# Optimization experiments

Hardware: AMD Instinct MI355X
Metric: run time of the kernel (lower is better)

Reference implementation:

```python
import jax, jax.numpy as jnp
import numpy as np
from jax import lax

N = 200; E = 3200; HID = 64; NH = 16; OUT = 2 * HID; CAT = NH * OUT  # CAT = 2048
ALPHA = 0.2


def _gat(h, e_attr, adj, n2n, W, a_s, a_d, a_e, We, concat):
    # edge-feature-aware GAT head: logits from Wh_i, Wh_j and projected node2node feats
    Nn = h.shape[0]
    Wh = h @ W                                       # [N, out]
    ee = ((n2n @ We) @ a_e).reshape(Nn, Nn)          # [N, N] edge-feature term
    logits = jax.nn.leaky_relu((Wh @ a_s)[:, None] + (Wh @ a_d)[None, :] + ee,
                               negative_slope=ALPHA)
    logits = jnp.where(adj > 0, logits, -1e9)        # mask to graph structure
    att = jax.nn.softmax(logits, axis=1)
    h2 = att @ Wh
    if concat:
        h2 = jax.nn.elu(h2)
    return h2, jax.nn.elu(e_attr @ We)               # updated node + edge features


def _edge_pool(x, eidx, e, w, b):
    # static-shape edge pooling: score edges, gate nodes by mean incident score
    src, dst = eidx[0], eidx[1]
    s = jax.nn.sigmoid(jnp.concatenate([x[src], x[dst], e], axis=1) @ w + b)  # [E]
    deg = jax.ops.segment_sum(jnp.ones_like(s), src, num_segments=x.shape[0])
    ns = jax.ops.segment_sum(s, src, num_segments=x.shape[0]) / (deg + 1e-6)
    return x * ns[:, None], e * s[:, None]


def _gpool(x, w, b):
    # GlobalAttention: gate_nn = Linear+Sigmoid, softmax over nodes, weighted sum
    gate = jax.nn.softmax(jax.nn.sigmoid(x @ w + b), axis=0)  # [N, 1]
    return jnp.sum(gate * x, axis=0, keepdims=True)           # [1, D]


def _adj_n2n(Nn, eidx, eattr):
    # vectorized version of the per-edge Python loop in _get_adj_node2node
    src, dst = eidx[0], eidx[1]
    adj = jnp.zeros((Nn, Nn), eattr.dtype).at[src, dst].set(1.0)
    n2n = jnp.zeros((Nn * Nn, eattr.shape[1]), eattr.dtype).at[src * Nn + dst].set(eattr)
    return adj, n2n


def _lstm_dir(x, Wih, Whh, b):
    # one LSTM direction over seq x [T, Din] (PyTorch i,f,g,o gate order)
    Hh = Whh.shape[1]
    def step(carry, xt):
        h, c = carry
        g = xt @ Wih.T + h @ Whh.T + b
        i, f, gg, o = jnp.split(g, 4)
        c = jax.nn.sigmoid(f) * c + jax.nn.sigmoid(i) * jnp.tanh(gg)
        h = jax.nn.sigmoid(o) * jnp.tanh(c)
        return (h, c), h
    (_, _), ys = lax.scan(step, (jnp.zeros(Hh, x.dtype), jnp.zeros(Hh, x.dtype)), x)
    return ys


def setup_inputs():
    key = jax.random.key(0)
    ks = iter(jax.random.split(key, 64))
    def rn(shape, scale=0.05):
        return jax.random.normal(next(ks), shape, jnp.float32) * scale
    inp = {}
    for g in (1, 2):
        eidx = jax.random.randint(next(ks), (2, E), 0, N)
        eattr = rn((E, HID), 1.0)
        adj, n2n = _adj_n2n(N, eidx, eattr)
        inp['features%d' % g] = rn((N, HID), 1.0)
        inp['edge_index%d' % g] = eidx
        inp['edgesAttr%d' % g] = eattr
        inp['adjacency%d' % g] = adj
        inp['node2node%d' % g] = n2n
    inp.update(dict(
        W_h=rn((HID, HID)),
        W_gat=rn((NH, HID, OUT)), a_src=rn((NH, OUT)), a_dst=rn((NH, OUT)),
        a_e=rn((NH, OUT)), We_gat=rn((NH, HID, OUT)),
        W_out=rn((CAT, OUT)), ao_src=rn((OUT,)), ao_dst=rn((OUT,)), ao_e=rn((OUT,)),
        We_out=rn((CAT, OUT)),
        ep1_w=rn((3 * CAT,)), ep1_b=rn(()),
        ep2_w=rn((3 * OUT,)), ep2_b=rn(()),
        g1_w=rn((HID, 1)), g1_b=rn((1,)),
        g2_w=rn((CAT, 1)), g2_b=rn((1,)),
        g3_w=rn((OUT, 1)), g3_b=rn((1,)),
        Wih0=rn((2, 512, 35 * HID)), Whh0=rn((2, 512, 128)), b0=rn((2, 512)),
        Wih1=rn((2, 512, 256)), Whh1=rn((2, 512, 128)), b1=rn((2, 512)),
        fc_w=rn((256, 2)), fc_b=rn((2,)),
    ))
    return inp


def reference(features1, features2, edge_index1, edge_index2, edgesAttr1, edgesAttr2,
              adjacency1, adjacency2, node2node1, node2node2,
              W_h, W_gat, a_src, a_dst, a_e, We_gat,
              W_out, ao_src, ao_dst, ao_e, We_out,
              ep1_w, ep1_b, ep2_w, ep2_b,
              g1_w, g1_b, g2_w, g2_b, g3_w, g3_b,
              Wih0, Whh0, b0, Wih1, Whh1, b1, fc_w, fc_b):
    def graph(feat, eidx, eattr, adj, n2n):
        h = jax.nn.elu(feat @ W_h)                              # SingleNodeAttentionLayer
        hs = [_gpool(h, g1_w, g1_b)]
        outs = [_gat(h, eattr, adj, n2n, W_gat[i], a_src[i], a_dst[i], a_e[i],
                     We_gat[i], True) for i in range(NH)]
        h = jnp.concatenate([o[0] for o in outs], axis=1)       # [N, 2048]
        eattr = jnp.concatenate([o[1] for o in outs], axis=1)   # [E, 2048]
        h, eattr = _edge_pool(h, eidx, eattr, ep1_w, ep1_b)
        hs.append(_gpool(h, g2_w, g2_b))
        adj2, n2n2 = _adj_n2n(h.shape[0], eidx, eattr)          # dense [N*N, 2048]
        h, eattr = _gat(h, eattr, adj2, n2n2, W_out, ao_src, ao_dst, ao_e, We_out, False)
        h, eattr = _edge_pool(h, eidx, eattr, ep2_w, ep2_b)
        hs.append(_gpool(h, g3_w, g3_b))
        return jnp.concatenate(hs, axis=1)                      # [1, 35*HID]

    h1 = graph(features1, edge_index1, edgesAttr1, adjacency1, node2node1)
    h2 = graph(features2, edge_index2, edgesAttr2, adjacency2, node2node2)
    x = jnp.concatenate([h1, h2], axis=0)                       # seq [2, 2240]
    for Wih, Whh, b in ((Wih0, Whh0, b0), (Wih1, Whh1, b1)):
        f = _lstm_dir(x, Wih[0], Whh[0], b[0])
        r = _lstm_dir(x[::-1], Wih[1], Whh[1], b[1])[::-1]
        x = jnp.concatenate([f, r], axis=1)                     # [2, 256]
    logits = x[-1] @ fc_w + fc_b
    return jax.nn.softmax(logits)[None, :]                      # [1, nclass]
```

## Files before the change

kernel.cpp:

```cpp
#include <hip/hip_runtime.h>
#include <math.h>

#define DI static __device__ __forceinline__

DI float eluf(float x){ return x > 0.f ? x : expm1f(x); }
DI float lreluf(float x){ return x > 0.f ? x : 0.2f*x; }
DI float sigmf(float x){ return 1.f/(1.f+expf(-x)); }

typedef unsigned short u16;
typedef unsigned int   u32;
typedef __attribute__((ext_vector_type(8))) short short8_t;
typedef __attribute__((ext_vector_type(4))) float f32x4;

DI u16 bf16rne(float f){
  u32 u = __float_as_uint(f);
  u += 0x7fffu + ((u>>16)&1u);
  return (u16)(u>>16);
}

DI f32x4 bmfma(short8_t a, short8_t b, f32x4 c){
  return __builtin_amdgcn_mfma_f32_16x16x32_bf16(a, b, c, 0, 0, 0);
}

constexpr int N=200, E=3200, HID=64, NH=16, OUTD=128, CAT=2048, SEQD=2240;

constexpr int OH0   = 0;
constexpr int OWH   = OH0 + N*HID;
constexpr int OASN  = OWH + NH*N*OUTD;
constexpr int OADN  = OASN + NH*N;
constexpr int OH1   = OADN + NH*N;
constexpr int OXW1  = OH1 + N*CAT;
constexpr int OXW2  = OXW1 + 256;
constexpr int OEW1  = OXW2 + 256;
constexpr int OS1   = OEW1 + E;
constexpr int ODEG1 = OS1 + E;
constexpr int OSS1  = ODEG1 + 256;
constexpr int ORAW1 = OSS1 + 256;
constexpr int OWH2  = ORAW1 + 256;
constexpr int OAS2  = OWH2 + N*OUTD;
constexpr int OAD2  = OAS2 + 256;
constexpr int OEWV  = OAD2 + 256;
constexpr int OH2B  = OEWV + E;
constexpr int OXS2  = OH2B + N*OUTD;
constexpr int OXD2  = OXS2 + 256;
constexpr int ODEG2 = OXD2 + 256;
constexpr int OSS2  = ODEG2 + 256;
constexpr int ORAW2 = OSS2 + 256;
constexpr int ORAW3 = ORAW2 + 256;
constexpr int PGF   = ORAW3 + 256;
constexpr int GLOBF = 10624;
constexpr int TOTF  = GLOBF + 2*PGF;

__device__ float G_F[TOTF];
__device__ float G_E2PART[(size_t)2*2*E*OUTD];
__device__ float G_EDOTH[2*NH*E];
__device__ float G_WHHT[2*2*128*512];
__device__ int   G_PIDX[2*N*N];
__device__ __attribute__((aligned(16))) u16 G_WGAT_T[NH*OUTD*HID];
__device__ __attribute__((aligned(16))) u16 G_WOUT_T[OUTD*CAT];
__device__ __attribute__((aligned(16))) u16 G_EATTR_BF[2*E*HID];

DI float* gf(int g){ return G_F + GLOBF + (size_t)g*PGF; }
DI float* gwe_ae(){ return G_F; }
DI float* gv_e(){ return G_F + 1024; }
DI float* gy0(){ return G_F + 3072; }
DI float* gy1(){ return G_F + 3584; }
DI float* gxseq(){ return G_F + 4096; }
DI float* gxg(){ return G_F + 8576; }
DI int*   gpidx(int g){ return G_PIDX + g*N*N; }

struct GraphIn {
  const float *feat, *eattr, *adj, *n2n;
  const int   *eidx;
};

struct Params {
  GraphIn g[2];
  const float *W_h, *W_gat, *a_src, *a_dst, *a_e, *We_gat;
  const float *W_out, *ao_src, *ao_dst, *ao_e, *We_out;
  const float *ep1_w, *ep1_b, *ep2_w, *ep2_b;
  const float *g1_w, *g1_b, *g2_w, *g2_b, *g3_w, *g3_b;
  const float *Wih0, *Whh0, *b0, *Wih1, *Whh1, *b1, *fc_w, *fc_b;
  float *out;
};

constexpr int ZPG  = 2*E + 1024;
constexpr int IB_Z = (2*ZPG+255)/256;
constexpr int IB_C = (2*N*N+255)/256;
constexpr int IB_D = (2*2*512*128)/256;
constexpr int IB_E = (NH*HID+CAT+3)/4;
constexpr int IB_H = (2*N+3)/4;
constexpr int IB_W1 = (NH*OUTD*HID)/256;
constexpr int IB_W2 = (OUTD*CAT)/256;
constexpr int IB_EA = (2*E*HID)/256;
__global__ void k_init(Params P){
  int b = blockIdx.x, tid = threadIdx.x;
  if (b < IB_Z){
    int i = b*256 + tid;
    if (i < 2*ZPG){
      int g = i/ZPG, r = i%ZPG;
      int addr = r<E ? OEW1+r : (r<2*E ? OEWV+(r-E) :
                 (r<2*E+512 ? ODEG1+(r-2*E) : ODEG2+(r-2*E-512)));
      gf(g)[addr] = 0.f;
    }
  } else if (b < IB_Z+IB_C){
    int i = (b-IB_Z)*256 + tid; if (i < 2*N*N) G_PIDX[i] = -1;
  } else if (b < IB_Z+IB_C+IB_D){
    int idx = (b-IB_Z-IB_C)*256 + tid;
    int l = idx >> 17;
    int r = idx & 131071;
    int d = r >> 16;
    int r2 = r & 65535;
    int gate = r2 & 511;
    int k = r2 >> 9;
    const float* Whh = l ? P.Whh1 : P.Whh0;
    G_WHHT[idx] = Whh[((size_t)d*512+gate)*128 + k];
  } else if (b < IB_Z+IB_C+IB_D+IB_E){
    int gid = (b-IB_Z-IB_C-IB_D)*4 + (tid>>6);
    int lane = tid & 63;
    if (gid < NH*HID){
      int h = gid/HID, c = gid%HID;
      const float* W = P.We_gat + (size_t)(h*HID+c)*OUTD;
      const float* a = P.a_e + h*OUTD;
      float acc = 0.f;
      for (int o=lane;o<OUTD;o+=64) acc += W[o]*a[o];
      for (int off=32;off>0;off>>=1) acc += __shfl_down(acc,off);
      if (lane==0) gwe_ae()[gid] = acc;
    } else if (gid < NH*HID+CAT){
      int c = gid - NH*HID;
      const float* W = P.We_out + (size_t)c*OUTD;
      float acc = 0.f;
      for (int o=lane;o<OUTD;o+=64) acc += W[o]*P.ao_e[o];
      for (int off=32;off>0;off>>=1) acc += __shfl_down(acc,off);
      if (lane==0) gv_e()[c] = acc;
    }
  } else if (b < IB_Z+IB_C+IB_D+IB_E+IB_H){
    int unit = (b-IB_Z-IB_C-IB_D-IB_E)*4 + (tid>>6);
    if (unit >= 2*N) return;
    int g = unit / N, n = unit % N, c = tid & 63;
    const float* feat = P.g[g].feat;
    float acc = 0.f;
    for (int k=0;k<HID;k++) acc += feat[n*HID+k]*P.W_h[k*HID+c];
    float v = eluf(acc);
    float* f = gf(g);
    f[OH0 + n*HID + c] = v;
    float r = v*P.g1_w[c];
    for (int off=32;off>0;off>>=1) r += __shfl_down(r,off);
    if (c==0) f[ORAW1+n] = r;
  } else if (b < IB_Z+IB_C+IB_D+IB_E+IB_H+IB_W1){
    int i = (b-(IB_Z+IB_C+IB_D+IB_E+IB_H))*256 + tid;
    int h = i>>13, o = (i>>6)&127, c = i&63;
    G_WGAT_T[i] = bf16rne(P.We_gat[(size_t)(h*HID+c)*OUTD + o]);
  } else if (b < IB_Z+IB_C+IB_D+IB_E+IB_H+IB_W1+IB_W2){
    int i = (b-(IB_Z+IB_C+IB_D+IB_E+IB_H+IB_W1))*256 + tid;
    int n = i>>11, q = i&2047;
    G_WOUT_T[i] = bf16rne(P.We_out[(size_t)q*OUTD + n]);
  } else {
    int i = (b-(IB_Z+IB_C+IB_D+IB_E+IB_H+IB_W1+IB_W2))*256 + tid;
    int g = i >= E*HID ? 1 : 0;
    G_EATTR_BF[i] = bf16rne(P.g[g].eattr[i - g*E*HID]);
  }
}

__global__ void k_edoth(Params P){
  int unit = blockIdx.x*4 + (threadIdx.x>>6);
  int lane = threadIdx.x & 63;
  int g = unit >= E ? 1 : 0;
  int e = unit - g*E;
  float val = P.g[g].eattr[(size_t)e*HID + lane];
  const float* wa = gwe_ae();
  float* eo = G_EDOTH + (size_t)g*NH*E + e;
  for (int h=0; h<NH; h++){
    float p = val * wa[h*HID + lane];
    for (int off=32; off>0; off>>=1) p += __shfl_down(p, off);
    if (lane==0) eo[(size_t)h*E] = p;
  }
}

__global__ void k_Wh(Params P){
  int n = blockIdx.x, h = blockIdx.y, g = blockIdx.z, o = threadIdx.x;
  float* f = gf(g);
  if (h == NH){
    if (n != 0) return;
    __shared__ float att[N];
    __shared__ float sb[128];
    for (int j = o; j < N; j += 128) att[j] = sigmf(f[ORAW1+j] + P.g1_b[0]);
    __syncthreads();
    float m = -3e38f;
    for (int j = o; j < N; j += 128) m = fmaxf(m, att[j]);
    sb[o] = m; __syncthreads();
    for (int s=64;s>0;s>>=1){ if (o<s) sb[o]=fmaxf(sb[o],sb[o+s]); __syncthreads(); }
    m = sb[0]; __syncthreads();
    float ss = 0.f;
    for (int j = o; j < N; j += 128){ float e = expf(att[j]-m); ss += e; }
    sb[o] = ss; __syncthreads();
    for (int s=64;s>0;s>>=1){ if (o<s) sb[o]+=sb[o+s]; __syncthreads(); }
    float inv = 1.f/sb[0]; __syncthreads();
    for (int j = o; j < N; j += 128) att[j] = expf(att[j]-m)*inv;
    __syncthreads();
    if (o < HID){
      float acc = 0.f;
      for (int j=0;j<N;j++) acc += att[j]*f[OH0 + j*HID + o];
      gxseq()[g*SEQD + o] = acc;
    }
    return;
  }
  __shared__ float hs[HID];
  __shared__ float sred[128], dred[128];
  if (o < HID) hs[o] = f[OH0 + n*HID + o];
  __syncthreads();
  const float* W = P.W_gat + (size_t)h*HID*OUTD + o;
  float acc = 0.f;
  for (int c=0;c<HID;c++) acc += hs[c]*W[(size_t)c*OUTD];
  f[OWH + ((size_t)h*N + n)*OUTD + o] = acc;
  sred[o] = acc*P.a_src[h*OUTD+o];
  dred[o] = acc*P.a_dst[h*OUTD+o];
  __syncthreads();
  for (int s=64;s>0;s>>=1){ if (o<s){ sred[o]+=sred[o+s]; dred[o]+=dred[o+s]; } __syncthreads(); }
  if (o==0){ f[OASN+h*N+n]=sred[0]; f[OADN+h*N+n]=dred[0]; }
}

__global__ void k_att1(Params P){
  int nb = blockIdx.x, h = blockIdx.y, g = blockIdx.z, tid = threadIdx.x;
  int n0 = nb*4;
  __shared__ float z[4][N];
  __shared__ float red[128];
  __shared__ float sinv[4];
  float* f = gf(g);
  const float* adj = P.g[g].adj;
  const int* pidx = gpidx(g);
  const float* edoth = G_EDOTH + ((size_t)g*NH + h)*E;
  const float* adn = f + OADN + h*N;
  for (int i=0;i<4;i++){
    float asn = f[OASN + h*N + n0+i];
    for (int j = tid; j < N; j += 128){
      float a = adj[(n0+i)*N + j];
      float zz;
      if (a > 0.f){
        int p = pidx[(n0+i)*N + j];
        float ee = (p >= 0) ? edoth[p] : 0.f;
        zz = lreluf(asn + adn[j] + ee);
      } else zz = -1e9f;
      z[i][j] = zz;
    }
  }
  __syncthreads();
  for (int i=0;i<4;i++){
    float m = -3e38f;
    for (int j = tid; j < N; j += 128) m = fmaxf(m, z[i][j]);
    red[tid] = m; __syncthreads();
    for (int s=64;s>0;s>>=1){ if (tid<s) red[tid]=fmaxf(red[tid],red[tid+s]); __syncthreads(); }
    m = red[0]; __syncthreads();
    float ssum = 0.f;
    for (int j = tid; j < N; j += 128){ float e = expf(z[i][j]-m); z[i][j]=e; ssum += e; }
    red[tid] = ssum; __syncthreads();
    for (int s=64;s>0;s>>=1){ if (tid<s) red[tid]+=red[tid+s]; __syncthreads(); }
    if (tid==0) sinv[i] = 1.f/red[0];
    __syncthreads();
  }
  const float* wh = f + OWH + (size_t)h*N*OUTD;
  float a0=0.f,a1=0.f,a2=0.f,a3=0.f;
  for (int j=0;j<N;j++){
    float w = wh[(size_t)j*OUTD + tid];
    a0 += z[0][j]*w; a1 += z[1][j]*w; a2 += z[2][j]*w; a3 += z[3][j]*w;
  }
  f[OH1 + (size_t)(n0+0)*CAT + h*OUTD + tid] = eluf(a0*sinv[0]);
  f[OH1 + (size_t)(n0+1)*CAT + h*OUTD + tid] = eluf(a1*sinv[1]);
  f[OH1 + (size_t)(n0+2)*CAT + h*OUTD + tid] = eluf(a2*sinv[2]);
  f[OH1 + (size_t)(n0+3)*CAT + h*OUTD + tid] = eluf(a3*sinv[3]);
}

__global__ void k_xw1(Params P){
  int n = blockIdx.x, g = blockIdx.y, tid = threadIdx.x;
  __shared__ float s1b[256], s2b[256], s3b[256];
  float* f = gf(g);
  const float* x = f + OH1 + (size_t)n*CAT;
  float a1 = 0.f, a2 = 0.f, a3 = 0.f;
  for (int c = tid; c < CAT; c += 256){
    float xv = x[c];
    a1 += xv*P.ep1_w[c];
    a2 += xv*P.ep1_w[CAT+c];
    a3 += xv*P.g2_w[c];
  }
  s1b[tid]=a1; s2b[tid]=a2; s3b[tid]=a3; __syncthreads();
  for (int s=128;s>0;s>>=1){
    if (tid<s){ s1b[tid]+=s1b[tid+s]; s2b[tid]+=s2b[tid+s]; s3b[tid]+=s3b[tid+s]; }
    __syncthreads();
  }
  if (tid==0){ f[OXW1+n]=s1b[0]; f[OXW2+n]=s2b[0]; f[ORAW2+n]=s3b[0]; }
}

__global__ void k_s1(Params P){
  int e = blockIdx.x*256 + threadIdx.x, g = blockIdx.y;
  if (e >= E) return;
  float* f = gf(g);
  const int* ei = P.g[g].eidx;
  int s = ei[e], d = ei[E+e];
  float v = sigmf(f[OXW1+s] + f[OXW2+d] + f[OEW1+e] + P.ep1_b[0]);
  f[OS1+e] = v;
  atomicAdd(&f[OSS1+s], v);
  atomicAdd(&f[ODEG1+s], 1.f);
}

__global__ void k_pairs(Params P){
  int e = blockIdx.x*256 + threadIdx.x, g = blockIdx.y;
  if (e >= E) return;
  const int* ei = P.g[g].eidx;
  atomicMax(&gpidx(g)[ei[e]*N + ei[E+e]], e);
}

__global__ void k_gpool_out(Params P, int xoff, int D, int odeg, int rawoff,
                            const float* b, int outoff){
  int cb = blockIdx.x, g = blockIdx.y, tid = threadIdx.x;
  __shared__ float att[N];
  __shared__ float sb[256];
  float* f = gf(g);
  for (int n = tid; n < N; n += 256){
    float sc = f[odeg+256+n]/(f[odeg+n]+1e-6f);
    att[n] = sigmf(f[rawoff+n]*sc + b[0]);
  }
  __syncthreads();
  float m = -3e38f;
  for (int n = tid; n < N; n += 256) m = fmaxf(m, att[n]);
  sb[tid] = m; __syncthreads();
  for (int s=128;s>0;s>>=1){ if (tid<s) sb[tid]=fmaxf(sb[tid],sb[tid+s]); __syncthreads(); }
  m = sb[0]; __syncthreads();
  float ss = 0.f;
  for (int n = tid; n < N; n += 256){ float e = expf(att[n]-m); ss += e; }
  sb[tid] = ss; __syncthreads();
  for (int s=128;s>0;s>>=1){ if (tid<s) sb[tid]+=sb[tid+s]; __syncthreads(); }
  float inv = 1.f/sb[0]; __syncthreads();
  for (int n = tid; n < N; n += 256){
    float sc = f[odeg+256+n]/(f[odeg+n]+1e-6f);
    att[n] = expf(att[n]-m)*inv*sc;
  }
  __syncthreads();
  int c = cb*256 + tid;
  if (c < D){
    const float* x = f + xoff;
    float acc = 0.f;
    for (int n=0;n<N;n++) acc += att[n]*x[(size_t)n*D + c];
    gxseq()[g*SEQD + outoff + c] = acc;
  }
}

__global__ void k_Wh2(Params P){
  int n = blockIdx.x, g = blockIdx.y, tid = threadIdx.x;
  int kq = tid >> 7, o = tid & 127;
  __shared__ float hrow[4][128];
  __shared__ float part[4][128];
  __shared__ float sr[128], dr[128];
  float* f = gf(g);
  const float* x = f + OH1 + (size_t)n*CAT;
  float acc = 0.f;
  for (int cc=0; cc<4; cc++){
    int c0 = kq*512 + cc*128;
    __syncthreads();
    hrow[kq][o] = x[c0 + o];
    __syncthreads();
    const float* W = P.W_out + (size_t)c0*OUTD + o;
    for (int j=0;j<128;j++) acc += hrow[kq][j]*W[(size_t)j*OUTD];
  }
  part[kq][o] = acc;
  __syncthreads();
  if (kq==0){
    float ns = f[OSS1+n]/(f[ODEG1+n]+1e-6f);
    float a = part[0][o]+part[1][o]+part[2][o]+part[3][o];
    float v = a*ns;
    f[OWH2 + (size_t)n*OUTD + o] = v;
    sr[o] = v*P.ao_src[o];
    dr[o] = v*P.ao_dst[o];
  }
  __syncthreads();
  for (int s=64;s>0;s>>=1){
    if (tid<s){ sr[tid]+=sr[tid+s]; dr[tid]+=dr[tid+s]; }
    __syncthreads();
  }
  if (tid==0){ f[OAS2+n]=sr[0]; f[OAD2+n]=dr[0]; }
}

__global__ void k_att2(Params P){
  int n = blockIdx.x, g = blockIdx.y, tid = threadIdx.x;
  __shared__ float z[N];
  __shared__ float red[128];
  __shared__ float dred[128];
  __shared__ float gred[128];
  float* f = gf(g);
  const float* adj = P.g[g].adj;
  const int* pidx = gpidx(g);
  float asn = f[OAS2+n];
  const float* adn = f + OAD2;
  for (int j = tid; j < N; j += 128){
    float a = adj[n*N + j];
    float zz;
    if (a > 0.f){
      int p = pidx[n*N + j];
      float ee = (p >= 0) ? f[OEWV+p]*f[OS1+p] : 0.f;
      zz = lreluf(asn + adn[j] + ee);
    } else zz = -1e9f;
    z[j] = zz;
  }
  __syncthreads();
  float m = -3e38f;
  for (int j = tid; j < N; j += 128) m = fmaxf(m, z[j]);
  red[tid] = m; __syncthreads();
  for (int s=64;s>0;s>>=1){ if (tid<s) red[tid]=fmaxf(red[tid],red[tid+s]); __syncthreads(); }
  m = red[0]; __syncthreads();
  float ssum = 0.f;
  for (int j = tid; j < N; j += 128){ float e = expf(z[j]-m); z[j]=e; ssum += e; }
  red[tid] = ssum; __syncthreads();
  for (int s=64;s>0;s>>=1){ if (tid<s) red[tid]+=red[tid+s]; __syncthreads(); }
  float inv = 1.f/red[0]; __syncthreads();
  const float* wh = f + OWH2;
  float acc = 0.f;
  for (int j=0;j<N;j++){
    float w = z[j];
    if (w != 0.f) acc += w * wh[(size_t)j*OUTD + tid];
  }
  float v = acc*inv;
  f[OH2B + (size_t)n*OUTD + tid] = v;
  red[tid]  = v*P.ep2_w[tid];
  dred[tid] = v*P.ep2_w[OUTD+tid];
  gred[tid] = v*P.g3_w[tid];
  __syncthreads();
  for (int s=64;s>0;s>>=1){
    if (tid<s){ red[tid]+=red[tid+s]; dred[tid]+=dred[tid+s]; gred[tid]+=gred[tid+s]; }
    __syncthreads();
  }
  if (tid==0){ f[OXS2+n]=red[0]; f[OXD2+n]=dred[0]; f[ORAW3+n]=gred[0]; }
}

__global__ __launch_bounds__(256) void k_e2p_mfma(Params P){
  int eb = blockIdx.x, hg = blockIdx.y, g = blockIdx.z;
  int tid = threadIdx.x;
  int wave = tid>>6, lane = tid&63, l16 = lane&15, l4 = lane>>4;
  __shared__ __attribute__((aligned(16))) u16 Tlds[16*512];
  int e0 = eb*16;
  int nt0 = wave*2;
  const u16* ea = G_EATTR_BF + ((size_t)g*E + e0)*HID;
  short8_t afrag0 = *(const short8_t*)(ea + l16*HID + l4*8);
  short8_t afrag1 = *(const short8_t*)(ea + l16*HID + 32 + l4*8);
  f32x4 acc0 = {0.f,0.f,0.f,0.f}, acc1 = {0.f,0.f,0.f,0.f};
  float ew1p[4] = {0.f,0.f,0.f,0.f};
  float ewvp[4] = {0.f,0.f,0.f,0.f};
  for (int pass=0; pass<2; pass++){
    if (pass) __syncthreads();
    for (int hh=0; hh<4; hh++){
      int h = hg*8 + pass*4 + hh;
      const u16* Wg = G_WGAT_T + (size_t)h*OUTD*HID;
      #pragma unroll
      for (int nn=0; nn<2; nn++){
        int nt = nt0 + nn;
        const u16* Wgn = Wg + (size_t)(nt*16 + l16)*HID + l4*8;
        f32x4 d = {0.f,0.f,0.f,0.f};
        d = bmfma(afrag0, *(const short8_t*)Wgn, d);
        d = bmfma(afrag1, *(const short8_t*)(Wgn+32), d);
        int qg = h*OUTD + nt*16 + l16;
        float w1 = P.ep1_w[2*CAT + qg];
        float wv = gv_e()[qg];
        int qloc = hh*128 + nt*16 + l16;
        #pragma unroll
        for (int r=0;r<4;r++){
          float v = d[r] > 0.f ? d[r] : expm1f(d[r]);
          ew1p[r] += v*w1;
          ewvp[r] += v*wv;
          float o = __shfl_xor(v, 1);
          if (!(lane&1)){
            u32 pk = (u32)bf16rne(v) | ((u32)bf16rne(o)<<16);
            int row = l4*4 + r;
            int byte = (row*1024 + qloc*2) ^ ((row&7)<<4);
            *(u32*)((char*)Tlds + byte) = pk;
          }
        }
      }
    }
    __syncthreads();
    const u16* Wo0 = G_WOUT_T + (size_t)(nt0*16 + l16)*CAT      + hg*1024 + pass*512 + l4*8;
    const u16* Wo1 = G_WOUT_T + (size_t)(nt0*16 + 16 + l16)*CAT + hg*1024 + pass*512 + l4*8;
    #pragma unroll 4
    for (int ks=0; ks<16; ks++){
      int byte = (l16*1024 + ks*64 + l4*16) ^ ((l16&7)<<4);
      short8_t af = *(const short8_t*)((const char*)Tlds + byte);
      acc0 = bmfma(af, *(const short8_t*)(Wo0 + ks*32), acc0);
      acc1 = bmfma(af, *(const short8_t*)(Wo1 + ks*32), acc1);
    }
  }
  float* f = gf(g);
  #pragma unroll
  for (int r=0;r<4;r++){
    float a = ew1p[r], b2 = ewvp[r];
    a += __shfl_xor(a, 1); b2 += __shfl_xor(b2, 1);
    a += __shfl_xor(a, 2); b2 += __shfl_xor(b2, 2);
    a += __shfl_xor(a, 4); b2 += __shfl_xor(b2, 4);
    a += __shfl_xor(a, 8); b2 += __shfl_xor(b2, 8);
    if (l16==0){
      int e = e0 + l4*4 + r;
      atomicAdd(&f[OEW1+e], a);
      atomicAdd(&f[OEWV+e], b2);
    }
  }
  float* dst = G_E2PART + (((size_t)hg*2 + g)*E + e0)*OUTD;
  #pragma unroll
  for (int r=0;r<4;r++){
    int e = l4*4 + r;
    dst[(size_t)e*OUTD + nt0*16 + l16]      = acc0[r];
    dst[(size_t)e*OUTD + nt0*16 + 16 + l16] = acc1[r];
  }
}

constexpr int TE2 = 16;
__global__ void k_ew2fin(Params P){
  int e0 = blockIdx.x*TE2, g = blockIdx.y, tid = threadIdx.x;
  __shared__ float lred[2][TE2];
  float* f = gf(g);
  float w2 = P.ep2_w[2*OUTD + tid];
  int lane = tid & 63, wvi = tid >> 6;
  for (int e=0;e<TE2;e++){
    const float* src = G_E2PART + ((size_t)g*E + e0 + e)*OUTD + tid;
    float a = 0.f;
    for (int h=0;h<2;h++) a += src[(size_t)h*2*E*OUTD];
    float v = eluf(f[OS1+e0+e]*a) * w2;
    for (int off=32;off>0;off>>=1) v += __shfl_down(v,off);
    if (lane==0) lred[wvi][e]=v;
  }
  __syncthreads();
  if (tid < TE2){
    int e = e0 + tid;
    float ew2 = lred[0][tid]+lred[1][tid];
    const int* ei = P.g[g].eidx;
    int s = ei[e], d = ei[E+e];
    float v = sigmf(f[OXS2+s] + f[OXD2+d] + ew2 + P.ep2_b[0]);
    atomicAdd(&f[OSS2+s], v);
    atomicAdd(&f[ODEG2+s], 1.f);
  }
}

__global__ void k_lstm_xg(Params P, int layer){
  int gid = blockIdx.x*4 + (threadIdx.x>>6);
  int lane = threadIdx.x & 63;
  int t = gid >> 10;
  int rem = gid & 1023;
  int d = rem >> 9;
  int gate = rem & 511;
  const float* Wih = layer ? P.Wih1 : P.Wih0;
  const float* bb  = layer ? P.b1   : P.b0;
  const float* xin = layer ? gy0()  : gxseq();
  int Din = layer ? 256 : SEQD;
  const float* x = xin + t*Din;
  const float* Wr = Wih + ((size_t)d*512 + gate)*Din;
  float acc = 0.f;
  for (int k=lane; k<Din; k+=64) acc += x[k]*Wr[k];
  for (int off=32; off>0; off>>=1) acc += __shfl_down(acc, off);
  if (lane==0) gxg()[(t*2 + d)*512 + gate] = acc + bb[d*512 + gate];
}

__global__ void k_lstm_rec(Params P, int layer){
  int d = blockIdx.x, tid = threadIdx.x;
  float* yout = layer ? gy1() : gy0();
  const float* T = G_WHHT + (size_t)(layer*2 + d)*128*512;
  __shared__ float h[128], c[128], gbuf[512];
  if (tid < 128){ h[tid]=0.f; c[tid]=0.f; }
  __syncthreads();
  for (int s=0;s<2;s++){
    int t = (d==0) ? s : 1-s;
    float acc = gxg()[(t*2 + d)*512 + tid];
    for (int k=0;k<128;k++) acc += h[k]*T[(size_t)k*512 + tid];
    gbuf[tid] = acc;
    __syncthreads();
    if (tid < 128){
      float ii = sigmf(gbuf[tid]);
      float ff = sigmf(gbuf[128+tid]);
      float gg = tanhf(gbuf[256+tid]);
      float oo = sigmf(gbuf[384+tid]);
      float cn = ff*c[tid] + ii*gg;
      c[tid] = cn;
      float hn = oo*tanhf(cn);
      h[tid] = hn;
      yout[t*256 + d*128 + tid] = hn;
    }
    __syncthreads();
  }
}

__global__ void k_final(Params P){
  int tid = threadIdx.x;
  __shared__ float sb[256], sb2[256];
  const float* x = gy1() + 256;
  sb[tid]  = x[tid]*P.fc_w[tid*2+0];
  sb2[tid] = x[tid]*P.fc_w[tid*2+1];
  __syncthreads();
  for (int s=128;s>0;s>>=1){ if (tid<s){ sb[tid]+=sb[tid+s]; sb2[tid]+=sb2[tid+s]; } __syncthreads(); }
  if (tid==0){
    float l0 = sb[0] + P.fc_b[0];
    float l1 = sb2[0] + P.fc_b[1];
    float m = fmaxf(l0,l1);
    float e0 = expf(l0-m), e1 = expf(l1-m), inv = 1.f/(e0+e1);
    P.out[0] = e0*inv;
    P.out[1] = e1*inv;
  }
}

extern "C" void kernel_launch(void* const* d_in, const int* in_sizes, int n_in,
                              void* d_out, int out_size, void* d_ws, size_t ws_size,
                              hipStream_t stream){
  Params P;
  for (int g=0; g<2; ++g){
    int b = g*5;
    P.g[g].feat  = (const float*)d_in[b+0];
    P.g[g].eidx  = (const int*)d_in[b+1];
    P.g[g].eattr = (const float*)d_in[b+2];
    P.g[g].adj   = (const float*)d_in[b+3];
    P.g[g].n2n   = (const float*)d_in[b+4];
  }
  P.W_h   = (const float*)d_in[10];
  P.W_gat = (const float*)d_in[11];
  P.a_src = (const float*)d_in[12];
  P.a_dst = (const float*)d_in[13];
  P.a_e   = (const float*)d_in[14];
  P.We_gat= (const float*)d_in[15];
  P.W_out = (const float*)d_in[16];
  P.ao_src= (const float*)d_in[17];
  P.ao_dst= (const float*)d_in[18];
  P.ao_e  = (const float*)d_in[19];
  P.We_out= (const float*)d_in[20];
  P.ep1_w = (const float*)d_in[21];
  P.ep1_b = (const float*)d_in[22];
  P.ep2_w = (const float*)d_in[23];
  P.ep2_b = (const float*)d_in[24];
  P.g1_w  = (const float*)d_in[25];
  P.g1_b  = (const float*)d_in[26];
  P.g2_w  = (const float*)d_in[27];
  P.g2_b  = (const float*)d_in[28];
  P.g3_w  = (const float*)d_in[29];
  P.g3_b  = (const float*)d_in[30];
  P.Wih0  = (const float*)d_in[31];
  P.Whh0  = (const float*)d_in[32];
  P.b0    = (const float*)d_in[33];
  P.Wih1  = (const float*)d_in[34];
  P.Whh1  = (const float*)d_in[35];
  P.b1    = (const float*)d_in[36];
  P.fc_w  = (const float*)d_in[37];
  P.fc_b  = (const float*)d_in[38];
  P.out   = (float*)d_out;

  k_init <<<dim3(IB_Z+IB_C+IB_D+IB_E+IB_H+IB_W1+IB_W2+IB_EA), 256, 0, stream>>>(P);
  k_pairs<<<dim3((E+255)/256,2), 256, 0, stream>>>(P);
  k_edoth<<<dim3(2*E/4), 256, 0, stream>>>(P);
  k_e2p_mfma<<<dim3(E/16, 2, 2), 256, 0, stream>>>(P);
  k_Wh   <<<dim3(N,NH+1,2), 128, 0, stream>>>(P);
  k_att1 <<<dim3(N/4,NH,2),128, 0, stream>>>(P);
  k_xw1  <<<dim3(N,2),    256, 0, stream>>>(P);
  k_s1   <<<dim3((E+255)/256,2), 256, 0, stream>>>(P);
  k_gpool_out<<<dim3(8,2), 256, 0, stream>>>(P, OH1, CAT, ODEG1, ORAW2, P.g2_b, HID);
  k_Wh2  <<<dim3(N,2),    512, 0, stream>>>(P);
  k_att2 <<<dim3(N,2),    128, 0, stream>>>(P);
  k_ew2fin<<<dim3(E/TE2,2),128, 0, stream>>>(P);
  k_gpool_out<<<dim3(1,2), 256, 0, stream>>>(P, OH2B, OUTD, ODEG2, ORAW3, P.g3_b, HID+CAT);

  k_lstm_xg <<<dim3(512), 256, 0, stream>>>(P, 0);
  k_lstm_rec<<<dim3(2),   512, 0, stream>>>(P, 0);
  k_lstm_xg <<<dim3(512), 256, 0, stream>>>(P, 1);
  k_lstm_rec<<<dim3(2),   512, 0, stream>>>(P, 1);
  k_final<<<dim3(1), 256, 0, stream>>>(P);
}
```

Measured before the change: 387.5 us.

## Retile edge projection MFMA kernel to 32 edges and 4 head groups

The edge-projection MFMA kernel now processes 32 edges per block over 4 head groups of 4 heads each, replacing 16 edges over 2 groups of 8. Each weight fragment is reused across two edge tiles, and the output-weight loads are register double-buffered ahead of the MFMAs. The partial-sum buffer grows to 4 slices, which the finalize kernel now sums. Separately, k_edoth is rewritten as a small LDS-tiled dot-product kernel in place of per-head wave shuffle reductions. The cost is a larger LDS footprint and more partial sums to write and reduce.

```diff
diff --git a/kernel.cpp b/kernel.cpp
--- a/kernel.cpp
+++ b/kernel.cpp
@@ -51,8 +51,8 @@
 constexpr int GLOBF = 10624;
 constexpr int TOTF  = GLOBF + 2*PGF;
 
-__device__ float G_F[TOTF];
-__device__ float G_E2PART[(size_t)2*2*E*OUTD];
+__device__ __attribute__((aligned(16))) float G_F[TOTF];
+__device__ float G_E2PART[(size_t)4*2*E*OUTD];
 __device__ float G_EDOTH[2*NH*E];
 __device__ float G_WHHT[2*2*128*512];
 __device__ int   G_PIDX[2*N*N];
@@ -163,18 +163,24 @@
 }
 
 __global__ void k_edoth(Params P){
-  int unit = blockIdx.x*4 + (threadIdx.x>>6);
-  int lane = threadIdx.x & 63;
-  int g = unit >= E ? 1 : 0;
-  int e = unit - g*E;
-  float val = P.g[g].eattr[(size_t)e*HID + lane];
-  const float* wa = gwe_ae();
-  float* eo = G_EDOTH + (size_t)g*NH*E + e;
-  for (int h=0; h<NH; h++){
-    float p = val * wa[h*HID + lane];
-    for (int off=32; off>0; off>>=1) p += __shfl_down(p, off);
-    if (lane==0) eo[(size_t)h*E] = p;
-  }
+  int b = blockIdx.x, tid = threadIdx.x;
+  int g = b / (E/16);
+  int e0 = (b % (E/16)) * 16;
+  __shared__ float ea[16][HID+1];
+  __shared__ float wa[16][HID+1];
+  {
+    int row = tid >> 4, c0 = (tid & 15)*4;
+    float4 v = *(const float4*)&P.g[g].eattr[(size_t)(e0+row)*HID + c0];
+    ea[row][c0]=v.x; ea[row][c0+1]=v.y; ea[row][c0+2]=v.z; ea[row][c0+3]=v.w;
+    float4 w = *(const float4*)&gwe_ae()[row*HID + c0];
+    wa[row][c0]=w.x; wa[row][c0+1]=w.y; wa[row][c0+2]=w.z; wa[row][c0+3]=w.w;
+  }
+  __syncthreads();
+  int h = tid >> 4, el = tid & 15;
+  float acc = 0.f;
+  #pragma unroll
+  for (int c=0;c<HID;c++) acc += ea[el][c]*wa[h][c];
+  G_EDOTH[((size_t)g*NH + h)*E + e0 + el] = acc;
 }
 
 __global__ void k_Wh(Params P){
@@ -434,77 +440,96 @@
   int eb = blockIdx.x, hg = blockIdx.y, g = blockIdx.z;
   int tid = threadIdx.x;
   int wave = tid>>6, lane = tid&63, l16 = lane&15, l4 = lane>>4;
-  __shared__ __attribute__((aligned(16))) u16 Tlds[16*512];
-  int e0 = eb*16;
+  __shared__ __attribute__((aligned(16))) u16 Tlds[32*512];
+  int e0 = eb*32;
   int nt0 = wave*2;
   const u16* ea = G_EATTR_BF + ((size_t)g*E + e0)*HID;
-  short8_t afrag0 = *(const short8_t*)(ea + l16*HID + l4*8);
-  short8_t afrag1 = *(const short8_t*)(ea + l16*HID + 32 + l4*8);
-  f32x4 acc0 = {0.f,0.f,0.f,0.f}, acc1 = {0.f,0.f,0.f,0.f};
-  float ew1p[4] = {0.f,0.f,0.f,0.f};
-  float ewvp[4] = {0.f,0.f,0.f,0.f};
-  for (int pass=0; pass<2; pass++){
-    if (pass) __syncthreads();
-    for (int hh=0; hh<4; hh++){
-      int h = hg*8 + pass*4 + hh;
-      const u16* Wg = G_WGAT_T + (size_t)h*OUTD*HID;
+  short8_t af00 = *(const short8_t*)(ea + l16*HID + l4*8);
+  short8_t af01 = *(const short8_t*)(ea + l16*HID + 32 + l4*8);
+  short8_t af10 = *(const short8_t*)(ea + (16+l16)*HID + l4*8);
+  short8_t af11 = *(const short8_t*)(ea + (16+l16)*HID + 32 + l4*8);
+  float ew1p0[4] = {0.f,0.f,0.f,0.f}, ewvp0[4] = {0.f,0.f,0.f,0.f};
+  float ew1p1[4] = {0.f,0.f,0.f,0.f}, ewvp1[4] = {0.f,0.f,0.f,0.f};
+  for (int hh=0; hh<4; hh++){
+    int h = hg*4 + hh;
+    const u16* Wg = G_WGAT_T + (size_t)h*OUTD*HID;
+    #pragma unroll
+    for (int nn=0; nn<2; nn++){
+      int nt = nt0 + nn;
+      const u16* Wgn = Wg + (size_t)(nt*16 + l16)*HID + l4*8;
+      short8_t wg0 = *(const short8_t*)Wgn;
+      short8_t wg1 = *(const short8_t*)(Wgn + 32);
+      f32x4 d0 = {0.f,0.f,0.f,0.f}, d1 = {0.f,0.f,0.f,0.f};
+      d0 = bmfma(af00, wg0, d0);
+      d1 = bmfma(af10, wg0, d1);
+      d0 = bmfma(af01, wg1, d0);
+      d1 = bmfma(af11, wg1, d1);
+      int qg = h*OUTD + nt*16 + l16;
+      float w1 = P.ep1_w[2*CAT + qg];
+      float wv = gv_e()[qg];
+      int qloc = hh*128 + nt*16 + l16;
       #pragma unroll
-      for (int nn=0; nn<2; nn++){
-        int nt = nt0 + nn;
-        const u16* Wgn = Wg + (size_t)(nt*16 + l16)*HID + l4*8;
-        f32x4 d = {0.f,0.f,0.f,0.f};
-        d = bmfma(afrag0, *(const short8_t*)Wgn, d);
-        d = bmfma(afrag1, *(const short8_t*)(Wgn+32), d);
-        int qg = h*OUTD + nt*16 + l16;
-        float w1 = P.ep1_w[2*CAT + qg];
-        float wv = gv_e()[qg];
-        int qloc = hh*128 + nt*16 + l16;
-        #pragma unroll
-        for (int r=0;r<4;r++){
-          float v = d[r] > 0.f ? d[r] : expm1f(d[r]);
-          ew1p[r] += v*w1;
-          ewvp[r] += v*wv;
-          float o = __shfl_xor(v, 1);
-          if (!(lane&1)){
-            u32 pk = (u32)bf16rne(v) | ((u32)bf16rne(o)<<16);
-            int row = l4*4 + r;
-            int byte = (row*1024 + qloc*2) ^ ((row&7)<<4);
-            *(u32*)((char*)Tlds + byte) = pk;
-          }
-        }
+      for (int r=0;r<4;r++){
+        float v0 = d0[r] > 0.f ? d0[r] : expm1f(d0[r]);
+        float v1 = d1[r] > 0.f ? d1[r] : expm1f(d1[r]);
+        ew1p0[r] += v0*w1; ewvp0[r] += v0*wv;
+        ew1p1[r] += v1*w1; ewvp1[r] += v1*wv;
+        int row = l4*4 + r;
+        int byt = (row*1024 + qloc*2) ^ ((row&7)<<4);
+        *(u16*)((char*)Tlds + byt) = bf16rne(v0);
+        *(u16*)((char*)Tlds + byt + 16384) = bf16rne(v1);
       }
     }
-    __syncthreads();
-    const u16* Wo0 = G_WOUT_T + (size_t)(nt0*16 + l16)*CAT      + hg*1024 + pass*512 + l4*8;
-    const u16* Wo1 = G_WOUT_T + (size_t)(nt0*16 + 16 + l16)*CAT + hg*1024 + pass*512 + l4*8;
-    #pragma unroll 4
-    for (int ks=0; ks<16; ks++){
-      int byte = (l16*1024 + ks*64 + l4*16) ^ ((l16&7)<<4);
-      short8_t af = *(const short8_t*)((const char*)Tlds + byte);
-      acc0 = bmfma(af, *(const short8_t*)(Wo0 + ks*32), acc0);
-      acc1 = bmfma(af, *(const short8_t*)(Wo1 + ks*32), acc1);
-    }
-  }
+  }
+  const u16* WoA = G_WOUT_T + (size_t)(wave*32 + l16)*CAT + hg*512 + l4*8;
+  const u16* WoB = WoA + 16*CAT;
+  short8_t w0a = *(const short8_t*)WoA;
+  short8_t w0b = *(const short8_t*)WoB;
+  short8_t w1a = *(const short8_t*)(WoA + 32);
+  short8_t w1b = *(const short8_t*)(WoB + 32);
   float* f = gf(g);
   #pragma unroll
   for (int r=0;r<4;r++){
-    float a = ew1p[r], b2 = ewvp[r];
-    a += __shfl_xor(a, 1); b2 += __shfl_xor(b2, 1);
-    a += __shfl_xor(a, 2); b2 += __shfl_xor(b2, 2);
-    a += __shfl_xor(a, 4); b2 += __shfl_xor(b2, 4);
-    a += __shfl_xor(a, 8); b2 += __shfl_xor(b2, 8);
+    float a0 = ew1p0[r], b0 = ewvp0[r], a1 = ew1p1[r], b1 = ewvp1[r];
+    a0 += __shfl_xor(a0,1); b0 += __shfl_xor(b0,1); a1 += __shfl_xor(a1,1); b1 += __shfl_xor(b1,1);
+    a0 += __shfl_xor(a0,2); b0 += __shfl_xor(b0,2); a1 += __shfl_xor(a1,2); b1 += __shfl_xor(b1,2);
+    a0 += __shfl_xor(a0,4); b0 += __shfl_xor(b0,4); a1 += __shfl_xor(a1,4); b1 += __shfl_xor(b1,4);
+    a0 += __shfl_xor(a0,8); b0 += __shfl_xor(b0,8); a1 += __shfl_xor(a1,8); b1 += __shfl_xor(b1,8);
     if (l16==0){
       int e = e0 + l4*4 + r;
-      atomicAdd(&f[OEW1+e], a);
-      atomicAdd(&f[OEWV+e], b2);
-    }
+      atomicAdd(&f[OEW1+e], a0);
+      atomicAdd(&f[OEWV+e], b0);
+      atomicAdd(&f[OEW1+e+16], a1);
+      atomicAdd(&f[OEWV+e+16], b1);
+    }
+  }
+  __syncthreads();
+  f32x4 acc00 = {0.f,0.f,0.f,0.f}, acc01 = {0.f,0.f,0.f,0.f};
+  f32x4 acc10 = {0.f,0.f,0.f,0.f}, acc11 = {0.f,0.f,0.f,0.f};
+  #pragma unroll
+  for (int ks=0; ks<16; ks++){
+    short8_t na = w0a, nb = w0b;
+    if (ks < 14){
+      na = *(const short8_t*)(WoA + (ks+2)*32);
+      nb = *(const short8_t*)(WoB + (ks+2)*32);
+    }
+    int byt = (l16*1024 + ks*64 + l4*16) ^ ((l16&7)<<4);
+    short8_t a0 = *(const short8_t*)((const char*)Tlds + byt);
+    short8_t a1 = *(const short8_t*)((const char*)Tlds + byt + 16384);
+    acc00 = bmfma(a0, w0a, acc00);
+    acc10 = bmfma(a1, w0a, acc10);
+    acc01 = bmfma(a0, w0b, acc01);
+    acc11 = bmfma(a1, w0b, acc11);
+    w0a = w1a; w0b = w1b; w1a = na; w1b = nb;
   }
   float* dst = G_E2PART + (((size_t)hg*2 + g)*E + e0)*OUTD;
   #pragma unroll
   for (int r=0;r<4;r++){
-    int e = l4*4 + r;
-    dst[(size_t)e*OUTD + nt0*16 + l16]      = acc0[r];
-    dst[(size_t)e*OUTD + nt0*16 + 16 + l16] = acc1[r];
+    int ee = l4*4 + r;
+    dst[(size_t)ee*OUTD + wave*32 + l16]      = acc00[r];
+    dst[(size_t)ee*OUTD + wave*32 + 16 + l16] = acc01[r];
+    dst[(size_t)(16+ee)*OUTD + wave*32 + l16]      = acc10[r];
+    dst[(size_t)(16+ee)*OUTD + wave*32 + 16 + l16] = acc11[r];
   }
 }
 
@@ -518,7 +543,7 @@
   for (int e=0;e<TE2;e++){
     const float* src = G_E2PART + ((size_t)g*E + e0 + e)*OUTD + tid;
     float a = 0.f;
-    for (int h=0;h<2;h++) a += src[(size_t)h*2*E*OUTD];
+    for (int h=0;h<4;h++) a += src[(size_t)h*2*E*OUTD];
     float v = eluf(f[OS1+e0+e]*a) * w2;
     for (int off=32;off>0;off>>=1) v += __shfl_down(v,off);
     if (lane==0) lred[wvi][e]=v;
@@ -645,8 +670,8 @@
 
   k_init <<<dim3(IB_Z+IB_C+IB_D+IB_E+IB_H+IB_W1+IB_W2+IB_EA), 256, 0, stream>>>(P);
   k_pairs<<<dim3((E+255)/256,2), 256, 0, stream>>>(P);
-  k_edoth<<<dim3(2*E/4), 256, 0, stream>>>(P);
-  k_e2p_mfma<<<dim3(E/16, 2, 2), 256, 0, stream>>>(P);
+  k_edoth<<<dim3(2*(E/16)), 256, 0, stream>>>(P);
+  k_e2p_mfma<<<dim3(E/32, 4, 2), 256, 0, stream>>>(P);
   k_Wh   <<<dim3(N,NH+1,2), 128, 0, stream>>>(P);
   k_att1 <<<dim3(N/4,NH,2),128, 0, stream>>>(P);
   k_xw1  <<<dim3(N,2),    256, 0, stream>>>(P);
```

Result: faster. 367.6 us (-5.1%).
